# Performance work log

Measured on AMD Instinct MI355X. Metric: run time of the kernel, lower is better.

The kernel has to match this reference:

```python
import jax, jax.numpy as jnp
import numpy as np

EMBED_DIM = 512
NUM_HEADS = 8
NUM_LAYERS = 2
LN_EPS = 1e-5


def setup_inputs() -> dict:
    key = jax.random.key(0)
    ks = jax.random.split(key, 12)
    B, S, E, L = 8, 1024, EMBED_DIM, NUM_LAYERS
    scale = 1.0 / np.sqrt(E)  # kaiming-ish init scale for 1x1 conv weights
    return {
        "x": jax.random.normal(ks[0], (B, S, E), jnp.float32),
        "adj": jax.random.uniform(ks[1], (S, S), jnp.float32),
        "Wq": jax.random.normal(ks[2], (L, E, E), jnp.float32) * scale,
        "bq": jnp.zeros((L, E), jnp.float32),
        "Wk": jax.random.normal(ks[3], (L, E, E), jnp.float32) * scale,
        "bk": jnp.zeros((L, E), jnp.float32),
        "Wv": jax.random.normal(ks[4], (L, E, E), jnp.float32) * scale,
        "bv": jnp.zeros((L, E), jnp.float32),
        "Wo": jax.random.normal(ks[5], (L, E, E), jnp.float32) * scale,
        "bo": jnp.zeros((L, E), jnp.float32),
        "gamma": jnp.ones((L, E), jnp.float32),
        "beta": jnp.zeros((L, E), jnp.float32),
    }


def _layer_norm(x, g, b):
    mu = jnp.mean(x, axis=-1, keepdims=True)
    var = jnp.mean(jnp.square(x - mu), axis=-1, keepdims=True)
    return (x - mu) * jax.lax.rsqrt(var + LN_EPS) * g + b


def reference(x, adj, Wq, bq, Wk, bk, Wv, bv, Wo, bo, gamma, beta):
    B, S, E = x.shape
    H = NUM_HEADS
    D = E // H
    inv_sqrt_d = 1.0 / np.sqrt(D)
    for l in range(Wq.shape[0]):
        # 1x1 Conv2d over channel dim == per-token linear: out_f = sum_e W[f,e] x_e + b_f
        q = (jnp.einsum('bse,fe->bsf', x, Wq[l]) + bq[l]).reshape(B, S, H, D).transpose(0, 2, 1, 3)
        k = (jnp.einsum('bse,fe->bsf', x, Wk[l]) + bk[l]).reshape(B, S, H, D).transpose(0, 2, 1, 3)
        v = (jnp.einsum('bse,fe->bsf', x, Wv[l]) + bv[l]).reshape(B, S, H, D).transpose(0, 2, 1, 3)
        # adjacency-gated scaled dot-product attention: multiplicative mask BEFORE softmax
        scores = jnp.einsum('bhqd,bhkd->bhqk', q, k) * inv_sqrt_d
        scores = scores * adj  # broadcast [S,S] over [B,H,S,S]
        attn = jax.nn.softmax(scores, axis=-1)
        out = jnp.einsum('bhqk,bhkd->bhqd', attn, v)
        out = out.transpose(0, 2, 1, 3).reshape(B, S, E)
        out = jnp.einsum('bse,fe->bsf', out, Wo[l]) + bo[l]
        x = _layer_norm(x + out, gamma[l], beta[l])
    return x
```

## Files before the change

kernel.cpp:

```cpp
#include <hip/hip_runtime.h>
#include <stdint.h>

typedef _Float16 f16;
typedef _Float16 f16x8 __attribute__((ext_vector_type(8)));
typedef _Float16 f16x4 __attribute__((ext_vector_type(4)));
typedef float f32x4 __attribute__((ext_vector_type(4)));

constexpr int EMB = 512;
constexpr int SEQ = 1024;
constexpr int NH = 8;
constexpr int DHEAD = 64;
constexpr int NTOK = 8192;

#define GAS __attribute__((address_space(1)))
#define LAS __attribute__((address_space(3)))

#if __has_builtin(__builtin_amdgcn_exp2f)
#define EXP2F(x) __builtin_amdgcn_exp2f(x)
#else
#define EXP2F(x) exp2f(x)
#endif

#define SCHED_BAR() __builtin_amdgcn_sched_barrier(0)

static __device__ __forceinline__ void gload_lds16(const void* g, void* l) {
  __builtin_amdgcn_global_load_lds((const GAS void*)g, (LAS void*)l, 16, 0, 0);
}


__global__ void k_pack_w(const float* __restrict__ Wq, const float* __restrict__ Wk,
                         const float* __restrict__ Wv, const float* __restrict__ Wo,
                         f16* __restrict__ wqkv, f16* __restrict__ wo) {
  int tid = blockIdx.x * 256 + threadIdx.x;
  if (tid < 2 * 1536 * 128) {
    int e4 = tid & 127;
    int f = (tid >> 7) % 1536;
    int l = tid / (128 * 1536);
    int part = f >> 9, fr = f & 511;
    const float* src = (part == 0 ? Wq : part == 1 ? Wk : Wv) + (size_t)l * EMB * EMB + (size_t)fr * EMB + e4 * 4;
    float4 v = *(const float4*)src;
    f16x4 hv = {(f16)v.x, (f16)v.y, (f16)v.z, (f16)v.w};
    *(f16x4*)(wqkv + ((size_t)l * 1536 + f) * EMB + e4 * 4) = hv;
  }
  if (tid < 2 * 512 * 128) {
    int e4 = tid & 127;
    int f = (tid >> 7) % 512;
    int l = tid / (128 * 512);
    float4 v = *(const float4*)(Wo + (size_t)l * EMB * EMB + (size_t)f * EMB + e4 * 4);
    f16x4 hv = {(f16)v.x, (f16)v.y, (f16)v.z, (f16)v.w};
    *(f16x4*)(wo + ((size_t)l * 512 + f) * EMB + e4 * 4) = hv;
  }
}

__global__ void k_pack_b(const float* __restrict__ bq, const float* __restrict__ bk,
                         const float* __restrict__ bv, float* __restrict__ bqkv) {
  int tid = blockIdx.x * 256 + threadIdx.x;
  if (tid < 2 * 1536) {
    int f = tid % 1536, l = tid / 1536;
    int part = f >> 9, fr = f & 511;
    bqkv[tid] = (part == 0 ? bq : part == 1 ? bk : bv)[l * EMB + fr];
  }
}

__global__ void k_cvt(const float* __restrict__ x, f16* __restrict__ out) {
  int i = (blockIdx.x * 256 + threadIdx.x) * 8;
  float4 a = *(const float4*)(x + i);
  float4 b = *(const float4*)(x + i + 4);
  f16x8 h = {(f16)a.x, (f16)a.y, (f16)a.z, (f16)a.w, (f16)b.x, (f16)b.y, (f16)b.z, (f16)b.w};
  *(f16x8*)(out + i) = h;
}

__global__ void k_pack_adjP(const float* __restrict__ adj, f16* __restrict__ adjP) {
  int tid = blockIdx.x * 256 + threadIdx.x;
  int lo = tid & 15, t = (tid >> 4) & 15, qrow = tid >> 8;
  const float c = 0.125f * 1.44269504088896f;
  const float* row = adj + (size_t)qrow * SEQ + t * 64 + lo;
  f16x4 v = {(f16)(row[0] * c), (f16)(row[16] * c), (f16)(row[32] * c), (f16)(row[48] * c)};
  *(f16x4*)(adjP + (size_t)tid * 4) = v;
}


template <int MODE, int BK>
__global__ __launch_bounds__(256) void k_gemm(const f16* __restrict__ A, const f16* __restrict__ Bw,
                                              const float* __restrict__ bias, f16* __restrict__ Uout,
                                              f16* __restrict__ Qo, f16* __restrict__ Ko,
                                              f16* __restrict__ Vt) {
  constexpr int CH = 128 * BK / 8;
  constexpr int NT = EMB / BK;
  __shared__ f16x8 sA[3][CH];
  __shared__ f16x8 sB[3][CH];
  const int tid = threadIdx.x;
  const int lane = tid & 63;
  const int lanelow = lane & 15, lanehi = lane >> 4;
  const int wave = tid >> 6;
  const int wm = wave >> 1, wn = wave & 1;
  const int flat = blockIdx.x;
  const int mt = (flat & 7) * 8 + ((flat >> 3) & 7);
  const int nt = flat >> 6;
  const int m0 = mt * 128, n0 = nt * 128;

  f32x4 acc[4][4] = {};

  const f16* aB = A + (size_t)m0 * EMB;
  const f16* bB = Bw + (size_t)n0 * EMB;

  int srow[4], scl[4];
#pragma unroll
  for (int p = 0; p < (BK == 64 ? 4 : 2); ++p) {
    int c = p * 256 + tid;
    if (BK == 64) {
      srow[p] = c >> 3;
      scl[p] = (c & 7) ^ (srow[p] & 7);
    } else {
      int R = c >> 3, sub = c & 7;
      srow[p] = R * 2 + (sub >> 2);
      scl[p] = (sub & 3) ^ (R & 3);
    }
  }

#define GSTAGE(ktv, bufv)                                                                     \
  {                                                                                           \
    _Pragma("unroll") for (int p = 0; p < (BK == 64 ? 4 : 2); ++p) {                          \
      int c = p * 256 + tid;                                                                  \
      gload_lds16(aB + (size_t)srow[p] * EMB + (ktv) + scl[p] * 8, (char*)sA[bufv] + c * 16); \
      gload_lds16(bB + (size_t)srow[p] * EMB + (ktv) + scl[p] * 8, (char*)sB[bufv] + c * 16); \
    }                                                                                         \
  }

  GSTAGE(0, 0);

  int cur = 0;
  for (int t = 0; t < NT; ++t) {
    const int nb = (cur == 2) ? 0 : cur + 1;
    if (t < NT - 1) GSTAGE((t + 1) * BK, nb);
    SCHED_BAR();
    if (t < NT - 1) {
      if (BK == 64) asm volatile("s_waitcnt vmcnt(8)");
      else          asm volatile("s_waitcnt vmcnt(4)");
    } else {
      asm volatile("s_waitcnt vmcnt(0)");
    }
    SCHED_BAR();
    __builtin_amdgcn_s_barrier();
    SCHED_BAR();

    const f16x8* sAc = sA[cur];
    const f16x8* sBc = sB[cur];
#pragma unroll
    for (int ks = 0; ks < BK / 32; ++ks) {
      f16x8 af[4], bf[4];
#pragma unroll
      for (int m = 0; m < 4; ++m) {
        int r = wm * 64 + m * 16 + lanelow;
        af[m] = (BK == 64) ? sAc[r * 8 + ((ks * 4 + lanehi) ^ (r & 7))]
                           : sAc[(r >> 1) * 8 + (r & 1) * 4 + (lanehi ^ ((r >> 1) & 3))];
      }
#pragma unroll
      for (int n = 0; n < 4; ++n) {
        int r = wn * 64 + n * 16 + lanelow;
        bf[n] = (BK == 64) ? sBc[r * 8 + ((ks * 4 + lanehi) ^ (r & 7))]
                           : sBc[(r >> 1) * 8 + (r & 1) * 4 + (lanehi ^ ((r >> 1) & 3))];
      }
      __builtin_amdgcn_s_setprio(1);
#pragma unroll
      for (int m = 0; m < 4; ++m)
#pragma unroll
        for (int n = 0; n < 4; ++n)
          acc[m][n] = __builtin_amdgcn_mfma_f32_16x16x32_f16(af[m], bf[n], acc[m][n], 0, 0, 0);
      __builtin_amdgcn_s_setprio(0);
    }
    cur = nb;
  }
#undef GSTAGE

#pragma unroll
  for (int n = 0; n < 4; ++n) {
    int col = n0 + wn * 64 + n * 16 + lanelow;
    float bv = bias[col];
    if (MODE == 1 && (col >> 9) == 2) {
      int fr = col & 511, hh = fr >> 6, d = fr & 63;
#pragma unroll
      for (int m = 0; m < 4; ++m) {
        int rbase = m0 + wm * 64 + m * 16 + lanehi * 4;
        int b = rbase >> 10, s = rbase & 1023;
        f16x4 pv = {(f16)(acc[m][n][0] + bv), (f16)(acc[m][n][1] + bv),
                    (f16)(acc[m][n][2] + bv), (f16)(acc[m][n][3] + bv)};
        *(f16x4*)(Vt + ((size_t)(b * NH + hh) * DHEAD + d) * SEQ + s) = pv;
      }
    } else {
#pragma unroll
      for (int m = 0; m < 4; ++m) {
        int rbase = m0 + wm * 64 + m * 16 + lanehi * 4;
#pragma unroll
        for (int j = 0; j < 4; ++j) {
          float v = acc[m][n][j] + bv;
          int row = rbase + j;
          if (MODE == 0) {
            Uout[(size_t)row * EMB + col] = (f16)v;
          } else {
            int part = col >> 9, fr = col & 511;
            int hh = fr >> 6, d = fr & 63;
            int b = row >> 10, s = row & 1023;
            int bh = b * NH + hh;
            if (part == 0)
              Qo[((size_t)bh * SEQ + s) * DHEAD + d] = (f16)v;
            else
              Ko[((size_t)bh * SEQ + s) * DHEAD + d] = (f16)v;
          }
        }
      }
    }
  }
}


__global__ __launch_bounds__(256) void k_attn(const f16* __restrict__ Q, const f16* __restrict__ K,
                                              const f16* __restrict__ Vt, const f16* __restrict__ adjP,
                                              f16* __restrict__ Ob) {
  __shared__ __align__(16) f16 sK[3][4096];
  __shared__ __align__(16) f16 sV[3][4096];
  __shared__ __align__(16) f16 Pl[4 * 1024];
  const int tid = threadIdx.x;
  const int lane = tid & 63;
  const int lanelow = lane & 15, lanehi = lane >> 4;
  const int wave = tid >> 6;
  f16* Plw = Pl + wave * 1024;

  const int flat = blockIdx.x;
  const int bh = (flat & 7) * 8 + ((flat >> 3) & 7);
  const int qblk = flat >> 6;
  const int b = bh >> 3, hh = bh & 7;
  const int q0 = qblk * 64 + wave * 16;

  const f16* Kbase = K + (size_t)bh * SEQ * DHEAD;
  const f16* Vbase = Vt + (size_t)bh * DHEAD * SEQ;

  const int c0 = tid, c1 = tid + 256;
  const int r0 = c0 >> 3, ch0 = (c0 & 7) ^ (r0 & 7);
  const int r1 = c1 >> 3, ch1 = (c1 & 7) ^ (r1 & 7);

#define STAGE(tv, bufv)                                                                   \
  {                                                                                       \
    const int kts = (tv)*64;                                                              \
    gload_lds16(Kbase + (size_t)(kts + r0) * DHEAD + ch0 * 8, (char*)sK[bufv] + c0 * 16); \
    gload_lds16(Kbase + (size_t)(kts + r1) * DHEAD + ch1 * 8, (char*)sK[bufv] + c1 * 16); \
    gload_lds16(Vbase + (size_t)r0 * SEQ + kts + ch0 * 8, (char*)sV[bufv] + c0 * 16);     \
    gload_lds16(Vbase + (size_t)r1 * SEQ + kts + ch1 * 8, (char*)sV[bufv] + c1 * 16);     \
  }

  f16x8 qf[2];
#pragma unroll
  for (int ks = 0; ks < 2; ++ks)
    qf[ks] = *(const f16x8*)(Q + ((size_t)bh * SEQ + q0 + lanelow) * DHEAD + ks * 32 + lanehi * 8);

  const f16* Ab = adjP + ((size_t)(q0 + lanehi * 4) * 256 + lanelow) * 4;
  f16x4 ab[4];
#define LOAD_A(tv)                                                           \
  {                                                                          \
    _Pragma("unroll") for (int j = 0; j < 4; ++j)                            \
        ab[j] = *(const f16x4*)(Ab + ((size_t)j * 256 + (tv)*16) * 4);       \
  }

  f32x4 oacc[4] = {};
  float lpart[4] = {};

  LOAD_A(0);
  SCHED_BAR();
  STAGE(0, 0);

  int cur = 0;
  for (int t = 0; t < 16; ++t) {
    const int nb = (cur == 2) ? 0 : cur + 1;

    f16x4 acur[4];
#pragma unroll
    for (int j = 0; j < 4; ++j) acur[j] = ab[j];

    if (t < 15) LOAD_A(t + 1);
    SCHED_BAR();
    if (t < 15) STAGE(t + 1, nb);
    SCHED_BAR();
    if (t < 15) asm volatile("s_waitcnt vmcnt(8)");
    else        asm volatile("s_waitcnt vmcnt(0)");
    SCHED_BAR();
    __builtin_amdgcn_s_barrier();
    SCHED_BAR();

    const f16* sKc = sK[cur];
    const f16* sVc = sV[cur];

    f32x4 sacc[4] = {};
#pragma unroll
    for (int ks = 0; ks < 2; ++ks) {
      f16x8 kf[4];
#pragma unroll
      for (int n = 0; n < 4; ++n) {
        int r = n * 16 + lanelow;
        kf[n] = *(const f16x8*)(sKc + (r * 8 + ((ks * 4 + lanehi) ^ (r & 7))) * 8);
      }
      __builtin_amdgcn_s_setprio(1);
#pragma unroll
      for (int n = 0; n < 4; ++n)
        sacc[n] = __builtin_amdgcn_mfma_f32_16x16x32_f16(qf[ks], kf[n], sacc[n], 0, 0, 0);
      __builtin_amdgcn_s_setprio(0);
    }

#pragma unroll
    for (int nh = 0; nh < 2; ++nh) {
#pragma unroll
      for (int j = 0; j < 4; ++j) {
        const int prow = lanehi * 4 + j;
        const f16x4 a4 = acur[j];
#pragma unroll
        for (int nn = 0; nn < 2; ++nn) {
          const int n = nh * 2 + nn;
          float p = EXP2F(sacc[n][j] * (float)a4[n]);
          lpart[j] += p;
          Plw[prow * 64 + (((n * 2 + (lanelow >> 3)) ^ (prow & 7)) * 8) + (lanelow & 7)] = (f16)p;
        }
      }
      f16x8 pa, vf[4];
      pa = *(const f16x8*)(Plw + lanelow * 64 + (((nh * 4 + lanehi) ^ (lanelow & 7)) * 8));
#pragma unroll
      for (int n = 0; n < 4; ++n) {
        int r = n * 16 + lanelow;
        vf[n] = *(const f16x8*)(sVc + (r * 8 + ((nh * 4 + lanehi) ^ (r & 7))) * 8);
      }
      __builtin_amdgcn_s_setprio(1);
#pragma unroll
      for (int n = 0; n < 4; ++n)
        oacc[n] = __builtin_amdgcn_mfma_f32_16x16x32_f16(pa, vf[n], oacc[n], 0, 0, 0);
      __builtin_amdgcn_s_setprio(0);
    }

    cur = nb;
  }
#undef STAGE
#undef LOAD_A

  float linv[4];
#pragma unroll
  for (int j = 0; j < 4; ++j) {
    float l = lpart[j];
#pragma unroll
    for (int off = 1; off < 16; off <<= 1) l += __shfl_xor(l, off, 16);
    linv[j] = 1.0f / l;
  }
#pragma unroll
  for (int n = 0; n < 4; ++n)
#pragma unroll
    for (int j = 0; j < 4; ++j) {
      int qrow = q0 + lanehi * 4 + j;
      float v = oacc[n][j] * linv[j];
      Ob[((size_t)b * SEQ + qrow) * EMB + hh * DHEAD + n * 16 + lanelow] = (f16)v;
    }
}


__global__ __launch_bounds__(256) void k_ln(const float* __restrict__ xin, const f16* __restrict__ Uin,
                                            const float* __restrict__ gamma, const float* __restrict__ beta,
                                            float* __restrict__ xout, f16* __restrict__ xh_out) {
  const int row = blockIdx.x * 4 + (threadIdx.x >> 6);
  const int lane = threadIdx.x & 63;
  const size_t base = (size_t)row * EMB + lane * 8;
  float u[8];
  {
    float4 a0 = *(const float4*)(xin + base);
    float4 a1 = *(const float4*)(xin + base + 4);
    f16x8 uh = *(const f16x8*)(Uin + base);
    u[0] = a0.x + (float)uh[0]; u[1] = a0.y + (float)uh[1];
    u[2] = a0.z + (float)uh[2]; u[3] = a0.w + (float)uh[3];
    u[4] = a1.x + (float)uh[4]; u[5] = a1.y + (float)uh[5];
    u[6] = a1.z + (float)uh[6]; u[7] = a1.w + (float)uh[7];
  }
  float s = 0.f;
#pragma unroll
  for (int i = 0; i < 8; ++i) s += u[i];
#pragma unroll
  for (int off = 1; off < 64; off <<= 1) s += __shfl_xor(s, off, 64);
  const float mu = s * (1.0f / EMB);
  float v = 0.f;
#pragma unroll
  for (int i = 0; i < 8; ++i) { float d = u[i] - mu; v += d * d; }
#pragma unroll
  for (int off = 1; off < 64; off <<= 1) v += __shfl_xor(v, off, 64);
  const float rs = rsqrtf(v * (1.0f / EMB) + 1e-5f);
  const int ci = lane * 8;
  float4 g0 = *(const float4*)(gamma + ci);
  float4 g1 = *(const float4*)(gamma + ci + 4);
  float4 b0 = *(const float4*)(beta + ci);
  float4 b1 = *(const float4*)(beta + ci + 4);
  float g[8] = {g0.x, g0.y, g0.z, g0.w, g1.x, g1.y, g1.z, g1.w};
  float be[8] = {b0.x, b0.y, b0.z, b0.w, b1.x, b1.y, b1.z, b1.w};
  float o[8];
#pragma unroll
  for (int i = 0; i < 8; ++i) o[i] = (u[i] - mu) * rs * g[i] + be[i];
  float4 o0 = {o[0], o[1], o[2], o[3]}, o1 = {o[4], o[5], o[6], o[7]};
  *(float4*)(xout + base) = o0;
  *(float4*)(xout + base + 4) = o1;
  if (xh_out) {
    f16x8 hv = {(f16)o[0], (f16)o[1], (f16)o[2], (f16)o[3], (f16)o[4], (f16)o[5], (f16)o[6], (f16)o[7]};
    *(f16x8*)(xh_out + base) = hv;
  }
}


extern "C" void kernel_launch(void* const* d_in, const int* in_sizes, int n_in,
                              void* d_out, int out_size, void* d_ws, size_t ws_size,
                              hipStream_t stream) {
  (void)in_sizes; (void)n_in; (void)out_size; (void)ws_size;
  const float* x = (const float*)d_in[0];
  const float* adj = (const float*)d_in[1];
  const float* Wq = (const float*)d_in[2];
  const float* bq = (const float*)d_in[3];
  const float* Wk = (const float*)d_in[4];
  const float* bk = (const float*)d_in[5];
  const float* Wv = (const float*)d_in[6];
  const float* bv = (const float*)d_in[7];
  const float* Wo = (const float*)d_in[8];
  const float* bo = (const float*)d_in[9];
  const float* gamma = (const float*)d_in[10];
  const float* beta = (const float*)d_in[11];

  char* ws = (char*)d_ws;
  size_t off = 0;
  auto alloc = [&](size_t bytes) {
    char* p = ws + off;
    off += (bytes + 255) & ~(size_t)255;
    return p;
  };
  f16* wqkv = (f16*)alloc((size_t)2 * 1536 * 512 * sizeof(f16));
  f16* wo = (f16*)alloc((size_t)2 * 512 * 512 * sizeof(f16));
  float* bqkv = (float*)alloc((size_t)2 * 1536 * sizeof(float));
  f16* adjP = (f16*)alloc((size_t)SEQ * SEQ * sizeof(f16));
  f16* xh = (f16*)alloc((size_t)NTOK * EMB * sizeof(f16));
  f16* Qb = (f16*)alloc((size_t)NTOK * EMB * sizeof(f16));
  f16* Kb = (f16*)alloc((size_t)NTOK * EMB * sizeof(f16));
  f16* Vtb = (f16*)alloc((size_t)NTOK * EMB * sizeof(f16));
  f16* Ob = (f16*)alloc((size_t)NTOK * EMB * sizeof(f16));
  f16* U = (f16*)alloc((size_t)NTOK * EMB * sizeof(f16));
  float* x1 = (float*)alloc((size_t)NTOK * EMB * sizeof(float));

  k_pack_w<<<1536, 256, 0, stream>>>(Wq, Wk, Wv, Wo, wqkv, wo);
  k_pack_b<<<12, 256, 0, stream>>>(bq, bk, bv, bqkv);
  k_pack_adjP<<<1024, 256, 0, stream>>>(adj, adjP);
  k_cvt<<<2048, 256, 0, stream>>>(x, xh);

  const float* xcur = x;
  for (int l = 0; l < 2; ++l) {
    k_gemm<1, 32><<<768, 256, 0, stream>>>(xh, wqkv + (size_t)l * 1536 * 512, bqkv + l * 1536,
                                           nullptr, Qb, Kb, Vtb);
    k_attn<<<1024, 256, 0, stream>>>(Qb, Kb, Vtb, adjP, Ob);
    k_gemm<0, 64><<<256, 256, 0, stream>>>(Ob, wo + (size_t)l * 512 * 512, bo + l * 512,
                                           U, nullptr, nullptr, nullptr);
    float* xnext = (l == 0) ? x1 : (float*)d_out;
    k_ln<<<2048, 256, 0, stream>>>(xcur, U, gamma + l * 512, beta + l * 512, xnext,
                                   (l == 0) ? xh : nullptr);
    xcur = xnext;
  }
}
```

Baseline: 186.5 us.

## Load K/V fragments directly from global memory instead of LDS staging

```diff
diff --git a/kernel.cpp b/kernel.cpp
--- a/kernel.cpp
+++ b/kernel.cpp
@@ -217,8 +217,6 @@
 __global__ __launch_bounds__(256) void k_attn(const f16* __restrict__ Q, const f16* __restrict__ K,
                                               const f16* __restrict__ Vt, const f16* __restrict__ adjP,
                                               f16* __restrict__ Ob) {
-  __shared__ __align__(16) f16 sK[3][4096];
-  __shared__ __align__(16) f16 sV[3][4096];
   __shared__ __align__(16) f16 Pl[4 * 1024];
   const int tid = threadIdx.x;
   const int lane = tid & 63;
@@ -232,21 +230,8 @@
   const int b = bh >> 3, hh = bh & 7;
   const int q0 = qblk * 64 + wave * 16;
 
-  const f16* Kbase = K + (size_t)bh * SEQ * DHEAD;
-  const f16* Vbase = Vt + (size_t)bh * DHEAD * SEQ;
-
-  const int c0 = tid, c1 = tid + 256;
-  const int r0 = c0 >> 3, ch0 = (c0 & 7) ^ (r0 & 7);
-  const int r1 = c1 >> 3, ch1 = (c1 & 7) ^ (r1 & 7);
-
-#define STAGE(tv, bufv)                                                                   \
-  {                                                                                       \
-    const int kts = (tv)*64;                                                              \
-    gload_lds16(Kbase + (size_t)(kts + r0) * DHEAD + ch0 * 8, (char*)sK[bufv] + c0 * 16); \
-    gload_lds16(Kbase + (size_t)(kts + r1) * DHEAD + ch1 * 8, (char*)sK[bufv] + c1 * 16); \
-    gload_lds16(Vbase + (size_t)r0 * SEQ + kts + ch0 * 8, (char*)sV[bufv] + c0 * 16);     \
-    gload_lds16(Vbase + (size_t)r1 * SEQ + kts + ch1 * 8, (char*)sV[bufv] + c1 * 16);     \
-  }
+  const f16* Kb = K + ((size_t)bh * SEQ + lanelow) * DHEAD + lanehi * 8;
+  const f16* Vb = Vt + ((size_t)bh * DHEAD + lanelow) * SEQ + lanehi * 8;
 
   f16x8 qf[2];
 #pragma unroll
@@ -265,77 +250,61 @@
   float lpart[4] = {};
 
   LOAD_A(0);
-  SCHED_BAR();
-  STAGE(0, 0);
-
-  int cur = 0;
+
+#pragma unroll 2
   for (int t = 0; t < 16; ++t) {
-    const int nb = (cur == 2) ? 0 : cur + 1;
+    const int kts = t * 64;
+
+    f16x8 kf[2][4];
+#pragma unroll
+    for (int ks = 0; ks < 2; ++ks)
+#pragma unroll
+      for (int n = 0; n < 4; ++n)
+        kf[ks][n] = *(const f16x8*)(Kb + (size_t)(kts + n * 16) * DHEAD + ks * 32);
+
+    f32x4 sacc[4] = {};
+    __builtin_amdgcn_s_setprio(1);
+#pragma unroll
+    for (int ks = 0; ks < 2; ++ks)
+#pragma unroll
+      for (int n = 0; n < 4; ++n)
+        sacc[n] = __builtin_amdgcn_mfma_f32_16x16x32_f16(qf[ks], kf[ks][n], sacc[n], 0, 0, 0);
+    __builtin_amdgcn_s_setprio(0);
+
+    f16x8 vf[2][4];
+#pragma unroll
+    for (int ks = 0; ks < 2; ++ks)
+#pragma unroll
+      for (int n = 0; n < 4; ++n)
+        vf[ks][n] = *(const f16x8*)(Vb + (size_t)(n * 16) * SEQ + kts + ks * 32);
 
     f16x4 acur[4];
 #pragma unroll
     for (int j = 0; j < 4; ++j) acur[j] = ab[j];
-
     if (t < 15) LOAD_A(t + 1);
-    SCHED_BAR();
-    if (t < 15) STAGE(t + 1, nb);
-    SCHED_BAR();
-    if (t < 15) asm volatile("s_waitcnt vmcnt(8)");
-    else        asm volatile("s_waitcnt vmcnt(0)");
-    SCHED_BAR();
-    __builtin_amdgcn_s_barrier();
-    SCHED_BAR();
-
-    const f16* sKc = sK[cur];
-    const f16* sVc = sV[cur];
-
-    f32x4 sacc[4] = {};
+
+#pragma unroll
+    for (int j = 0; j < 4; ++j) {
+      const int prow = lanehi * 4 + j;
+      const f16x4 a4 = acur[j];
+#pragma unroll
+      for (int n = 0; n < 4; ++n) {
+        float p = EXP2F(sacc[n][j] * (float)a4[n]);
+        lpart[j] += p;
+        Plw[prow * 64 + (((n * 2 + (lanelow >> 3)) ^ (prow & 7)) * 8) + (lanelow & 7)] = (f16)p;
+      }
+    }
+
 #pragma unroll
     for (int ks = 0; ks < 2; ++ks) {
-      f16x8 kf[4];
-#pragma unroll
-      for (int n = 0; n < 4; ++n) {
-        int r = n * 16 + lanelow;
-        kf[n] = *(const f16x8*)(sKc + (r * 8 + ((ks * 4 + lanehi) ^ (r & 7))) * 8);
-      }
+      f16x8 pa = *(const f16x8*)(Plw + lanelow * 64 + (((ks * 4 + lanehi) ^ (lanelow & 7)) * 8));
       __builtin_amdgcn_s_setprio(1);
 #pragma unroll
       for (int n = 0; n < 4; ++n)
-        sacc[n] = __builtin_amdgcn_mfma_f32_16x16x32_f16(qf[ks], kf[n], sacc[n], 0, 0, 0);
+        oacc[n] = __builtin_amdgcn_mfma_f32_16x16x32_f16(pa, vf[ks][n], oacc[n], 0, 0, 0);
       __builtin_amdgcn_s_setprio(0);
     }
-
-#pragma unroll
-    for (int nh = 0; nh < 2; ++nh) {
-#pragma unroll
-      for (int j = 0; j < 4; ++j) {
-        const int prow = lanehi * 4 + j;
-        const f16x4 a4 = acur[j];
-#pragma unroll
-        for (int nn = 0; nn < 2; ++nn) {
-          const int n = nh * 2 + nn;
-          float p = EXP2F(sacc[n][j] * (float)a4[n]);
-          lpart[j] += p;
-          Plw[prow * 64 + (((n * 2 + (lanelow >> 3)) ^ (prow & 7)) * 8) + (lanelow & 7)] = (f16)p;
-        }
-      }
-      f16x8 pa, vf[4];
-      pa = *(const f16x8*)(Plw + lanelow * 64 + (((nh * 4 + lanehi) ^ (lanelow & 7)) * 8));
-#pragma unroll
-      for (int n = 0; n < 4; ++n) {
-        int r = n * 16 + lanelow;
-        vf[n] = *(const f16x8*)(sVc + (r * 8 + ((nh * 4 + lanehi) ^ (r & 7))) * 8);
-      }
-      __builtin_amdgcn_s_setprio(1);
-#pragma unroll
-      for (int n = 0; n < 4; ++n)
-        oacc[n] = __builtin_amdgcn_mfma_f32_16x16x32_f16(pa, vf[n], oacc[n], 0, 0, 0);
-      __builtin_amdgcn_s_setprio(0);
-    }
-
-    cur = nb;
-  }
-#undef STAGE
+  }
 #undef LOAD_A
 
   float linv[4];
```

Result: slower. 341.0 us (+82.8%).
